# Kernel optimization log

Hardware: AMD Instinct MI355X
Metric: run time of the kernel (lower is better)

## Reference

```python
import jax, jax.numpy as jnp
import numpy as np

N, E, DIN, DOUT, NNZ = 8192, 4096, 256, 128, 65536
TEMP = float(DOUT) ** 0.5
NEG = -1e9


def setup_inputs() -> dict:
    key = jax.random.key(0)
    ks = jax.random.split(key, 8)
    stdv = 1.0 / np.sqrt(DOUT)
    u = lambda k, shp: jax.random.uniform(k, shp, jnp.float32, -stdv, stdv)
    x = jax.random.normal(ks[0], (N, DIN), jnp.float32)
    nodes = jax.random.randint(ks[1], (NNZ,), 0, N, jnp.int32)
    edges = jax.random.randint(ks[2], (NNZ,), 0, E, jnp.int32)
    hyperedge_index = jnp.stack([nodes, edges])  # [2, nnz]
    return {
        "x": x,
        "weight": u(ks[3], (DIN, DOUT)),   # transfer weight
        "weight2": u(ks[4], (DIN, DOUT)),
        "weight3": u(ks[5], (DOUT, DOUT)),
        "bias": u(ks[6], (DOUT,)),
        "q_ctx": u(ks[7], (DOUT,)),        # word_context.weight[0]
        "hyperedge_index": hyperedge_index,
        "num_nodes": N,
        "num_edges": E,
    }


def reference(x, weight, weight2, weight3, bias, q_ctx, hyperedge_index, num_nodes, num_edges):
    # dense incidence H[node, edge] = 1  (hyperedge_preprocess)
    H = jnp.zeros((num_nodes, num_edges), x.dtype).at[
        hyperedge_index[0], hyperedge_index[1]].set(1.0)
    adj = H.T                       # [E, N]  (mask / original attention for attn1)

    x4 = x @ weight2                # [N, D]  x_4att
    xt = x @ weight + bias          # [N, D]  transferred features (v of attn1)

    # ---- attention1: query = shared word-context vector, keys = x4 ----
    row = (q_ctx / TEMP) @ x4.T                    # [N] (q1 rows are identical)
    scores1 = jnp.where(adj == 0, NEG, row[None, :])  # [E, N]
    att1 = jax.nn.softmax(adj, axis=-1) + jax.nn.softmax(scores1, axis=-1)
    edge = att1 @ xt                               # [E, D]

    att2he = att1.T                                # [N, E]

    # ---- attention2: queries = x4, keys = edge @ W3 ----
    edge4 = edge @ weight3                         # [E, D]
    scores2 = jnp.where(adj.T == 0, NEG, (x4 / TEMP) @ edge4.T)  # [N, E]
    att2hn = jax.nn.softmax(adj.T, axis=-1) + jax.nn.softmax(scores2, axis=-1)

    # ---- fused outer-product attention and output projection ----
    A = att2he @ att2he.T + att2hn @ att2hn.T      # [N, N]
    h_prime_g = jax.nn.elu(A @ x4)                 # [N, D]
    return h_prime_g
```

## Files before the change

kernel.cpp:

```cpp
#include <hip/hip_runtime.h>
#include <math.h>

constexpr int Nn   = 8192;
constexpr int Ee   = 4096;
constexpr int DIN  = 256;
constexpr int DOUT = 128;
constexpr int NNZ  = 65536;
constexpr int EC   = 96;
constexpr int NC   = 48;

#define TEMPR 0.08838834764831845f
#define EM1   1.7182818284590452f

typedef __attribute__((ext_vector_type(8))) short short8;
typedef __attribute__((ext_vector_type(4))) float f32x4;

static __device__ __forceinline__ float wave_sum64(float v) {
#pragma unroll
    for (int m = 32; m; m >>= 1) v += __shfl_xor(v, m, 64);
    return v;
}
static __device__ __forceinline__ float wave_max64(float v) {
#pragma unroll
    for (int m = 32; m; m >>= 1) v = fmaxf(v, __shfl_xor(v, m, 64));
    return v;
}
static __device__ __forceinline__ short f2bf(float f) {
    union { float f; unsigned u; } v; v.f = f;
    const unsigned r = (v.u + 0x7FFFu + ((v.u >> 16) & 1u)) >> 16;
    return (short)r;
}
static __device__ __forceinline__ unsigned packbf2(float a, float b) {
    return ((unsigned)(unsigned short)f2bf(a)) |
           (((unsigned)(unsigned short)f2bf(b)) << 16);
}
static __device__ __forceinline__ float2 unpackbf2(unsigned u) {
    union { unsigned u; float f; } lo, hi;
    lo.u = u << 16; hi.u = u & 0xFFFF0000u;
    return make_float2(lo.f, hi.f);
}

__global__ __launch_bounds__(256) void k_ww3(
    const float* __restrict__ W, const float* __restrict__ W2,
    const float* __restrict__ W3, const float* __restrict__ bias,
    short* __restrict__ W2T, short* __restrict__ WWT, float* __restrict__ bW3,
    uint4* __restrict__ zb, unsigned zTot16)
{
    const int b = blockIdx.x;
    const int t = threadIdx.x;
    if (b < 32) {
        __shared__ float sW[8][128];
        const int r0 = b * 8;
        for (int i = t; i < 1024; i += 256)
            sW[i >> 7][i & 127] = W[(size_t)(r0 + (i >> 7)) * DOUT + (i & 127)];
        __syncthreads();
        const int c  = t & 127;
        const int rh = (t >> 7) * 4;
        float acc[4] = {0.f, 0.f, 0.f, 0.f};
        for (int k = 0; k < 128; ++k) {
            const float w3 = W3[(size_t)k * DOUT + c];
#pragma unroll
            for (int i = 0; i < 4; ++i) acc[i] = fmaf(sW[rh + i][k], w3, acc[i]);
        }
#pragma unroll
        for (int i = 0; i < 4; ++i)
            WWT[(size_t)c * DIN + (r0 + rh + i)] = f2bf(acc[i]);
    } else if (b < 40) {
        const int k0 = (b - 32) * 32;
        for (int i = t; i < 32 * 128; i += 256) {
            const int k = k0 + (i >> 7);
            const int n = i & 127;
            W2T[(size_t)n * DIN + k] = f2bf(W2[(size_t)k * DOUT + n]);
        }
    } else if (b == 40) {
        if (t < 128) {
            float acc = 0.f;
            for (int k = 0; k < 128; ++k)
                acc = fmaf(bias[k], W3[(size_t)k * DOUT + t], acc);
            bW3[t] = acc;
        }
    } else {
        uint4 z; z.x = z.y = z.z = z.w = 0u;
        for (unsigned i = (unsigned)(b - 41) * 256u + t; i < zTot16;
             i += 64u * 256u)
            zb[i] = z;
    }
}

__global__ __launch_bounds__(256) void k_gemm1f(
    const float* __restrict__ x, const short* __restrict__ W2T,
    const short* __restrict__ WWT, const float* __restrict__ bW3,
    const float* __restrict__ q, const int* __restrict__ hidx,
    unsigned* __restrict__ bitmap, int* __restrict__ degE, int* __restrict__ degN,
    int* __restrict__ csrEn, int* __restrict__ csrNe, int* __restrict__ csrNs,
    short* __restrict__ x4b, short* __restrict__ xwb,
    float* __restrict__ rowv)
{
    __shared__ float srow[16];
    const int t    = threadIdx.x;
    const int lane = t & 63;
    const int wv   = t >> 6;
    const int n16  = lane & 15;
    const int quad = lane >> 4;
    const int r0   = blockIdx.x * 16;
    const int n0   = wv * 32;

    const unsigned gid = blockIdx.x * 256 + t;
    if (gid < NNZ) {
        const int n = hidx[gid];
        const int e = hidx[NNZ + gid];
        const unsigned word = (unsigned)n * (unsigned)Ee + (unsigned)e;
        const unsigned bit  = 1u << (word & 31u);
        const unsigned old  = atomicOr(&bitmap[word >> 5], bit);
        if (!(old & bit)) {
            const int pe = atomicAdd(&degE[e], 1);
            if (pe < EC) {
                csrEn[e * EC + pe] = n;
                const int pn = atomicAdd(&degN[n], 1);
                if (pn < NC) {
                    csrNe[n * NC + pn] = e;
                    csrNs[n * NC + pn] = e * EC + pe;
                }
            }
        }
    }

    f32x4 acc4[2], accw[2];
#pragma unroll
    for (int nt = 0; nt < 2; ++nt) {
        acc4[nt] = (f32x4){0.f, 0.f, 0.f, 0.f};
        accw[nt] = (f32x4){0.f, 0.f, 0.f, 0.f};
    }
#pragma unroll
    for (int k0 = 0; k0 < DIN; k0 += 32) {
        const int kb = k0 + quad * 8;
        const float4 xa = *(const float4*)&x[(size_t)(r0 + n16) * DIN + kb];
        const float4 xb = *(const float4*)&x[(size_t)(r0 + n16) * DIN + kb + 4];
        short8 af;
        af[0] = f2bf(xa.x); af[1] = f2bf(xa.y); af[2] = f2bf(xa.z); af[3] = f2bf(xa.w);
        af[4] = f2bf(xb.x); af[5] = f2bf(xb.y); af[6] = f2bf(xb.z); af[7] = f2bf(xb.w);
#pragma unroll
        for (int nt = 0; nt < 2; ++nt) {
            const int col = n0 + nt * 16 + n16;
            const short8 b4 = *(const short8*)&W2T[(size_t)col * DIN + kb];
            const short8 bw = *(const short8*)&WWT[(size_t)col * DIN + kb];
            acc4[nt] = __builtin_amdgcn_mfma_f32_16x16x32_bf16(af, b4, acc4[nt], 0, 0, 0);
            accw[nt] = __builtin_amdgcn_mfma_f32_16x16x32_bf16(af, bw, accw[nt], 0, 0, 0);
        }
    }

    float bwv[2], qv[2];
#pragma unroll
    for (int nt = 0; nt < 2; ++nt) {
        const int col = n0 + nt * 16 + n16;
        bwv[nt] = bW3[col];
        qv[nt]  = q[col];
    }
#pragma unroll
    for (int nt = 0; nt < 2; ++nt) {
        const int col = n0 + nt * 16 + n16;
#pragma unroll
        for (int reg = 0; reg < 4; ++reg) {
            const int row = r0 + quad * 4 + reg;
            x4b[(size_t)row * DOUT + col] = f2bf(acc4[nt][reg]);
            xwb[(size_t)row * DOUT + col] = f2bf(accw[nt][reg] + bwv[nt]);
        }
    }
    float pr[4];
#pragma unroll
    for (int reg = 0; reg < 4; ++reg)
        pr[reg] = qv[0] * acc4[0][reg] + qv[1] * acc4[1][reg];
#pragma unroll
    for (int m = 8; m; m >>= 1) {
#pragma unroll
        for (int reg = 0; reg < 4; ++reg) pr[reg] += __shfl_xor(pr[reg], m, 64);
    }
    if (t < 16) srow[t] = 0.f;
    __syncthreads();
    if (n16 == 0) {
#pragma unroll
        for (int reg = 0; reg < 4; ++reg) atomicAdd(&srow[quad * 4 + reg], pr[reg]);
    }
    __syncthreads();
    if (t < 16) rowv[r0 + t] = srow[t] * TEMPR;
}

__global__ __launch_bounds__(256) void k_reduxA(
    const unsigned* __restrict__ x4b, const unsigned* __restrict__ xwb,
    const int* __restrict__ degE,
    float* __restrict__ csx4, float* __restrict__ csxw, float* __restrict__ c2g)
{
    const int t    = threadIdx.x;
    const int lane = t & 63;
    const int w    = t >> 6;
    const int b    = blockIdx.x;
    float2 a4 = {0.f, 0.f}, aw = {0.f, 0.f};
    for (int k = 0; k < 32; ++k) {
        const int n = b * 128 + w + k * 4;
        const float2 fv = unpackbf2(x4b[(size_t)n * 64 + lane]);
        const float2 tv = unpackbf2(xwb[(size_t)n * 64 + lane]);
        a4.x += fv.x; a4.y += fv.y;
        aw.x += tv.x; aw.y += tv.y;
    }
    atomicAdd(&csx4[lane * 2 + 0], a4.x); atomicAdd(&csx4[lane * 2 + 1], a4.y);
    atomicAdd(&csxw[lane * 2 + 0], aw.x); atomicAdd(&csxw[lane * 2 + 1], aw.y);

    const int gid = b * 256 + t;
    if (gid < Ee) {
        const int de = min(degE[gid], EC);
        const float ue = de ? 1.0f / ((float)Nn + (float)de * EM1)
                            : 2.0f / (float)Nn;
        const float v = wave_sum64(ue * ue);
        if (lane == 0) atomicAdd(c2g, v);
    }
}

__global__ __launch_bounds__(256) void k_edge1(
    const int* __restrict__ degE, const int* __restrict__ csrEn,
    const float* __restrict__ rowv,
    const float* __restrict__ csx4, const float* __restrict__ csxw,
    const unsigned* __restrict__ x4b, const unsigned* __restrict__ xwb,
    float* __restrict__ Sval, unsigned* __restrict__ e4b, unsigned* __restrict__ G1b,
    float* __restrict__ wsArr)
{
    __shared__ int   sN[4][EC];
    __shared__ float sS[4][EC];
    const int t    = threadIdx.x;
    const int w    = t >> 6;
    const int lane = t & 63;
    const int e    = blockIdx.x * 4 + w;
    const int deg  = min(degE[e], EC);
    const float ue = deg ? 1.0f / ((float)Nn + (float)deg * EM1) : 2.0f / (float)Nn;

    int   n0 = 0, n1 = 0;
    float r0 = -INFINITY, r1 = -INFINITY;
    if (lane < deg)      { n0 = csrEn[e * EC + lane];      r0 = rowv[n0]; }
    if (lane + 64 < deg) { n1 = csrEn[e * EC + lane + 64]; r1 = rowv[n1]; }
    const float m  = wave_max64(fmaxf(r0, r1));
    const float e0 = (lane < deg)      ? expf(r0 - m) : 0.f;
    const float e1 = (lane + 64 < deg) ? expf(r1 - m) : 0.f;
    const float Z  = wave_sum64(e0 + e1);
    const float inv = deg ? 1.0f / Z : 0.f;
    const float base = EM1 * ue;
    if (lane < deg) {
        const float sv = fmaf(e0, inv, base);
        sN[w][lane] = n0; sS[w][lane] = sv;
        Sval[e * EC + lane] = sv;
        atomicAdd(&wsArr[n0], ue * sv);
    }
    if (lane + 64 < deg) {
        const float sv = fmaf(e1, inv, base);
        sN[w][lane + 64] = n1; sS[w][lane + 64] = sv;
        Sval[e * EC + lane + 64] = sv;
        atomicAdd(&wsArr[n1], ue * sv);
    }

    const float2 cw = *(const float2*)&csxw[lane * 2];
    const float2 c4 = *(const float2*)&csx4[lane * 2];
    float2 aE = make_float2(ue * cw.x, ue * cw.y);
    float2 aG = make_float2(ue * c4.x, ue * c4.y);
    int j = 0;
    for (; j + 8 <= deg; j += 8) {
        int ai[8]; float bi[8]; unsigned tu[8], fu[8];
#pragma unroll
        for (int k = 0; k < 8; ++k) { ai[k] = sN[w][j+k]; bi[k] = sS[w][j+k]; }
#pragma unroll
        for (int k = 0; k < 8; ++k) {
            tu[k] = xwb[(size_t)ai[k] * 64 + lane];
            fu[k] = x4b[(size_t)ai[k] * 64 + lane];
        }
#pragma unroll
        for (int k = 0; k < 8; ++k) {
            const float2 tv = unpackbf2(tu[k]);
            const float2 fv = unpackbf2(fu[k]);
            aE.x = fmaf(bi[k], tv.x, aE.x); aE.y = fmaf(bi[k], tv.y, aE.y);
            aG.x = fmaf(bi[k], fv.x, aG.x); aG.y = fmaf(bi[k], fv.y, aG.y);
        }
    }
    for (; j < deg; ++j) {
        const int   a = sN[w][j];
        const float b = sS[w][j];
        const float2 tv = unpackbf2(xwb[(size_t)a * 64 + lane]);
        const float2 fv = unpackbf2(x4b[(size_t)a * 64 + lane]);
        aE.x = fmaf(b, tv.x, aE.x); aE.y = fmaf(b, tv.y, aE.y);
        aG.x = fmaf(b, fv.x, aG.x); aG.y = fmaf(b, fv.y, aG.y);
    }
    e4b[(size_t)e * 64 + lane] = packbf2(aE.x, aE.y);
    G1b[(size_t)e * 64 + lane] = packbf2(aG.x, aG.y);
}

__global__ __launch_bounds__(256) void k_reduxB(
    const unsigned* __restrict__ x4b, const int* __restrict__ degN,
    const float* __restrict__ wsArr,
    float* __restrict__ vxg, float* __restrict__ twxg, float* __restrict__ wsxg)
{
    const int t    = threadIdx.x;
    const int lane = t & 63;
    const int w    = t >> 6;
    const int b    = blockIdx.x;
    float2 av = {0.f, 0.f}, at2 = {0.f, 0.f}, aw = {0.f, 0.f};
    for (int k = 0; k < 32; ++k) {
        const int n   = b * 128 + w + k * 4;
        const int deg = min(degN[n], NC);
        const float vn = deg ? 1.0f / ((float)Ee + (float)deg * EM1) : 2.0f / (float)Ee;
        const float tw = deg ? fmaf((float)deg * EM1, vn, 1.0f) : 0.f;
        const float wsn = wsArr[n];
        const float2 xv = unpackbf2(x4b[(size_t)n * 64 + lane]);
        av.x  = fmaf(vn,  xv.x, av.x);  av.y  = fmaf(vn,  xv.y, av.y);
        at2.x = fmaf(tw,  xv.x, at2.x); at2.y = fmaf(tw,  xv.y, at2.y);
        aw.x  = fmaf(wsn, xv.x, aw.x);  aw.y  = fmaf(wsn, xv.y, aw.y);
    }
    atomicAdd(&vxg[lane * 2 + 0],  av.x);  atomicAdd(&vxg[lane * 2 + 1],  av.y);
    atomicAdd(&twxg[lane * 2 + 0], at2.x); atomicAdd(&twxg[lane * 2 + 1], at2.y);
    atomicAdd(&wsxg[lane * 2 + 0], aw.x);  atomicAdd(&wsxg[lane * 2 + 1], aw.y);
}

__global__ __launch_bounds__(256) void k_node2(
    const int* __restrict__ degN, const int* __restrict__ csrNe,
    const int* __restrict__ csrNs, const unsigned* __restrict__ x4b,
    const unsigned* __restrict__ e4b,
    float* __restrict__ Tval)
{
    const int t    = threadIdx.x;
    const int w    = t >> 6;
    const int lane = t & 63;
    const int es   = lane >> 3;
    const int dl   = lane & 7;
    const int n    = blockIdx.x * 4 + w;
    const int deg  = min(degN[n], NC);
    if (!deg) return;
    const float vn = 1.0f / ((float)Ee + (float)deg * EM1);

    const uint4* xr = (const uint4*)&x4b[(size_t)n * 64];
    const uint4 xua = xr[dl * 2], xub = xr[dl * 2 + 1];
    const float2 x0 = unpackbf2(xua.x), x1 = unpackbf2(xua.y),
                 x2 = unpackbf2(xua.z), x3 = unpackbf2(xua.w),
                 x4v = unpackbf2(xub.x), x5 = unpackbf2(xub.y),
                 x6 = unpackbf2(xub.z), x7 = unpackbf2(xub.w);

    float dps[6]; float exs[6]; int slots[6];
    float m = -INFINITY;
#pragma unroll
    for (int p = 0; p < 6; ++p) {
        dps[p] = -INFINITY; slots[p] = 0;
        if (p * 8 >= deg) continue;
        const int j = p * 8 + es;
        int ej = 0;
        if (j < deg) { ej = csrNe[n * NC + j]; slots[p] = csrNs[n * NC + j]; }
        const uint4* er = (const uint4*)&e4b[(size_t)ej * 64];
        const uint4 ea = er[dl * 2], eb = er[dl * 2 + 1];
        float d0 = 0.f, d1 = 0.f, d2 = 0.f, d3 = 0.f;
        { const float2 ev = unpackbf2(ea.x); d0 = fmaf(ev.x, x0.x, d0); d0 = fmaf(ev.y, x0.y, d0); }
        { const float2 ev = unpackbf2(ea.y); d1 = fmaf(ev.x, x1.x, d1); d1 = fmaf(ev.y, x1.y, d1); }
        { const float2 ev = unpackbf2(ea.z); d2 = fmaf(ev.x, x2.x, d2); d2 = fmaf(ev.y, x2.y, d2); }
        { const float2 ev = unpackbf2(ea.w); d3 = fmaf(ev.x, x3.x, d3); d3 = fmaf(ev.y, x3.y, d3); }
        { const float2 ev = unpackbf2(eb.x); d0 = fmaf(ev.x, x4v.x, d0); d0 = fmaf(ev.y, x4v.y, d0); }
        { const float2 ev = unpackbf2(eb.y); d1 = fmaf(ev.x, x5.x, d1); d1 = fmaf(ev.y, x5.y, d1); }
        { const float2 ev = unpackbf2(eb.z); d2 = fmaf(ev.x, x6.x, d2); d2 = fmaf(ev.y, x6.y, d2); }
        { const float2 ev = unpackbf2(eb.w); d3 = fmaf(ev.x, x7.x, d3); d3 = fmaf(ev.y, x7.y, d3); }
        float dot = (d0 + d1) + (d2 + d3);
        dot += __shfl_xor(dot, 1, 64);
        dot += __shfl_xor(dot, 2, 64);
        dot += __shfl_xor(dot, 4, 64);
        dot = (j < deg) ? dot * TEMPR : -INFINITY;
        dps[p] = dot;
        float mm = fmaxf(dot, __shfl_xor(dot, 8, 64));
        mm = fmaxf(mm, __shfl_xor(mm, 16, 64));
        mm = fmaxf(mm, __shfl_xor(mm, 32, 64));
        m = fmaxf(m, mm);
    }
    float Z = 0.f;
#pragma unroll
    for (int p = 0; p < 6; ++p) {
        exs[p] = 0.f;
        if (p * 8 >= deg) continue;
        const float ex = (p * 8 + es < deg) ? expf(dps[p] - m) : 0.f;
        exs[p] = ex;
        float s = ex + __shfl_xor(ex, 8, 64);
        s += __shfl_xor(s, 16, 64);
        s += __shfl_xor(s, 32, 64);
        Z += s;
    }
    const float invZ = 1.0f / Z;
#pragma unroll
    for (int p = 0; p < 6; ++p) {
        if (p * 8 >= deg) continue;
        if (dl == 0 && p * 8 + es < deg)
            Tval[slots[p]] = fmaf(EM1, vn, exs[p] * invZ);
    }
}

__global__ __launch_bounds__(256) void k_g2(
    const int* __restrict__ degE, const int* __restrict__ csrEn,
    const float* __restrict__ Tval, const float* __restrict__ vxg,
    const unsigned* __restrict__ x4b, unsigned* __restrict__ G2b)
{
    const int t    = threadIdx.x;
    const int w    = t >> 6;
    const int lane = t & 63;
    const int e    = blockIdx.x * 4 + w;
    const int deg  = min(degE[e], EC);
    float2 acc = *(const float2*)&vxg[lane * 2];
    int j = 0;
    for (; j + 8 <= deg; j += 8) {
        int ai[8]; float bi[8]; unsigned fu[8];
#pragma unroll
        for (int k = 0; k < 8; ++k) { ai[k] = csrEn[e*EC+j+k]; bi[k] = Tval[e*EC+j+k]; }
#pragma unroll
        for (int k = 0; k < 8; ++k)
            fu[k] = x4b[(size_t)ai[k] * 64 + lane];
#pragma unroll
        for (int k = 0; k < 8; ++k) {
            const float2 fv = unpackbf2(fu[k]);
            acc.x = fmaf(bi[k], fv.x, acc.x); acc.y = fmaf(bi[k], fv.y, acc.y);
        }
    }
    for (; j < deg; ++j) {
        const int   a = csrEn[e*EC+j];
        const float b = Tval[e*EC+j];
        const float2 fv = unpackbf2(x4b[(size_t)a * 64 + lane]);
        acc.x = fmaf(b, fv.x, acc.x); acc.y = fmaf(b, fv.y, acc.y);
    }
    G2b[(size_t)e * 64 + lane] = packbf2(acc.x, acc.y);
}

__global__ __launch_bounds__(256) void k_final(
    const int* __restrict__ degN, const int* __restrict__ csrNe,
    const int* __restrict__ csrNs, const float* __restrict__ Sval,
    const float* __restrict__ Tval,
    const float* __restrict__ c2g, const float* __restrict__ csx4,
    const float* __restrict__ wsxg, const float* __restrict__ vxg,
    const float* __restrict__ twxg,
    const unsigned* __restrict__ G1b, const unsigned* __restrict__ G2b,
    float* __restrict__ out)
{
    const int t    = threadIdx.x;
    const int w    = t >> 6;
    const int lane = t & 63;
    const int n    = blockIdx.x * 4 + w;
    const int deg  = min(degN[n], NC);
    const float vn = deg ? 1.0f / ((float)Ee + (float)deg * EM1) : 2.0f / (float)Ee;
    const float c2 = *c2g;
    const float2 c4v = *(const float2*)&csx4[lane * 2];
    const float2 wsv = *(const float2*)&wsxg[lane * 2];
    const float2 vxv = *(const float2*)&vxg[lane * 2];
    const float2 twv = *(const float2*)&twxg[lane * 2];
    float2 acc;
    acc.x = fmaf(c2, c4v.x, wsv.x) + vn * fmaf((float)Ee, vxv.x, twv.x);
    acc.y = fmaf(c2, c4v.y, wsv.y) + vn * fmaf((float)Ee, vxv.y, twv.y);
    int j = 0;
    for (; j + 4 <= deg; j += 4) {
        int ei[4], si[4]; float sv[4], tv[4]; unsigned g1u[4], g2u[4];
#pragma unroll
        for (int k = 0; k < 4; ++k) {
            ei[k] = csrNe[n*NC+j+k]; si[k] = csrNs[n*NC+j+k];
        }
#pragma unroll
        for (int k = 0; k < 4; ++k) {
            sv[k] = Sval[si[k]]; tv[k] = Tval[si[k]];
            g1u[k] = G1b[(size_t)ei[k] * 64 + lane];
            g2u[k] = G2b[(size_t)ei[k] * 64 + lane];
        }
#pragma unroll
        for (int k = 0; k < 4; ++k) {
            const float2 g1 = unpackbf2(g1u[k]);
            const float2 g2 = unpackbf2(g2u[k]);
            acc.x = fmaf(sv[k], g1.x, acc.x); acc.y = fmaf(sv[k], g1.y, acc.y);
            acc.x = fmaf(tv[k], g2.x, acc.x); acc.y = fmaf(tv[k], g2.y, acc.y);
        }
    }
    for (; j < deg; ++j) {
        const int ea = csrNe[n*NC+j];
        const int sa = csrNs[n*NC+j];
        const float sva = Sval[sa], tva = Tval[sa];
        const float2 g1a = unpackbf2(G1b[(size_t)ea * 64 + lane]);
        const float2 g2a = unpackbf2(G2b[(size_t)ea * 64 + lane]);
        acc.x = fmaf(sva, g1a.x, acc.x); acc.y = fmaf(sva, g1a.y, acc.y);
        acc.x = fmaf(tva, g2a.x, acc.x); acc.y = fmaf(tva, g2a.y, acc.y);
    }
    acc.x = acc.x > 0.f ? acc.x : expm1f(acc.x);
    acc.y = acc.y > 0.f ? acc.y : expm1f(acc.y);
    *(float2*)&out[(size_t)n * DOUT + lane * 2] = acc;
}

extern "C" void kernel_launch(void* const* d_in, const int* in_sizes, int n_in,
                              void* d_out, int out_size, void* d_ws, size_t ws_size,
                              hipStream_t stream)
{
    const float* x    = (const float*)d_in[0];
    const float* W    = (const float*)d_in[1];
    const float* W2   = (const float*)d_in[2];
    const float* W3   = (const float*)d_in[3];
    const float* bias = (const float*)d_in[4];
    const float* q    = (const float*)d_in[5];
    const int*   hidx = (const int*)d_in[6];
    float* out = (float*)d_out;

    char* wsp = (char*)d_ws;
    size_t o = 0;
    auto take = [&](size_t bytes) {
        size_t r = o; o += (bytes + 255) & ~(size_t)255; return r;
    };
    unsigned* bitmap = (unsigned*)(wsp + take((size_t)Nn * Ee / 8));
    int*   degE  = (int*)  (wsp + take((size_t)Ee * 4));
    int*   degN  = (int*)  (wsp + take((size_t)Nn * 4));
    float* wsArr = (float*)(wsp + take((size_t)Nn * 4));
    float* c2g   = (float*)(wsp + take(4));
    float* csx4  = (float*)(wsp + take(DOUT * 4));
    float* csxw  = (float*)(wsp + take(DOUT * 4));
    float* vxg   = (float*)(wsp + take(DOUT * 4));
    float* twxg  = (float*)(wsp + take(DOUT * 4));
    float* wsxg  = (float*)(wsp + take(DOUT * 4));
    const size_t zbytes = o;
    short* x4b   = (short*)(wsp + take((size_t)Nn * DOUT * 2));
    short* xwb   = (short*)(wsp + take((size_t)Nn * DOUT * 2));
    float* rowv  = (float*)(wsp + take((size_t)Nn * 4));
    int*   csrEn = (int*)  (wsp + take((size_t)Ee * EC * 4));
    float* Sval  = (float*)(wsp + take((size_t)Ee * EC * 4));
    float* Tval  = (float*)(wsp + take((size_t)Ee * EC * 4));
    int*   csrNe = (int*)  (wsp + take((size_t)Nn * NC * 4));
    int*   csrNs = (int*)  (wsp + take((size_t)Nn * NC * 4));
    unsigned* e4b = (unsigned*)(wsp + take((size_t)Ee * DOUT * 2));
    unsigned* G1b = (unsigned*)(wsp + take((size_t)Ee * DOUT * 2));
    unsigned* G2b = (unsigned*)(wsp + take((size_t)Ee * DOUT * 2));
    short* W2T   = (short*)(wsp + take((size_t)DOUT * DIN * 2));
    short* WWT   = (short*)(wsp + take((size_t)DOUT * DIN * 2));
    float* bW3   = (float*)(wsp + take(DOUT * 4));
    (void)ws_size; (void)in_sizes; (void)n_in; (void)out_size;

    k_ww3   <<<105,     256, 0, stream>>>(W, W2, W3, bias, W2T, WWT, bW3,
                                          (uint4*)d_ws, (unsigned)(zbytes / 16));
    k_gemm1f<<<Nn / 16, 256, 0, stream>>>(x, W2T, WWT, bW3, q, hidx,
                                          bitmap, degE, degN, csrEn, csrNe, csrNs,
                                          x4b, xwb, rowv);
    k_reduxA<<<64,      256, 0, stream>>>((const unsigned*)x4b, (const unsigned*)xwb,
                                          degE, csx4, csxw, c2g);
    k_edge1 <<<Ee / 4,  256, 0, stream>>>(degE, csrEn, rowv, csx4, csxw,
                                          (const unsigned*)x4b, (const unsigned*)xwb,
                                          Sval, e4b, G1b, wsArr);
    k_reduxB<<<64,      256, 0, stream>>>((const unsigned*)x4b, degN, wsArr,
                                          vxg, twxg, wsxg);
    k_node2 <<<Nn / 4,  256, 0, stream>>>(degN, csrNe, csrNs,
                                          (const unsigned*)x4b, e4b, Tval);
    k_g2    <<<Ee / 4,  256, 0, stream>>>(degE, csrEn, Tval, vxg,
                                          (const unsigned*)x4b, G2b);
    k_final <<<Nn / 4,  256, 0, stream>>>(degN, csrNe, csrNs, Sval, Tval,
                                          c2g, csx4, wsxg, vxg, twxg, G1b, G2b, out);
}
```

Baseline: 167.1 us.

## Interleave per-slot and per-row arrays into packed structs and merge reduction kernel

Packs the separate node-index, S and T arrays into one int4 per edge slot, and the node CSR edge/slot pair into an int2. It interleaves x4 and xw bf16 rows, and G1 and G2, so each gather fetches one 8-byte word instead of two 4-byte loads. The column order is permuted so the GEMM epilogue can pack adjacent outputs, and k_final un-permutes the layout on store. It also folds the k_reduxB reduction into the k_nodeB launch as extra blocks and deepens the edge gather unroll to 16. The intent is fewer scattered memory transactions and one fewer launch, at the cost of wider per-slot records and a duplicated x4 copy.

```diff
diff --git a/kernel.cpp b/kernel.cpp
--- a/kernel.cpp
+++ b/kernel.cpp
@@ -11,6 +11,7 @@
 
 #define TEMPR 0.08838834764831845f
 #define EM1   1.7182818284590452f
+
 
 typedef __attribute__((ext_vector_type(8))) short short8;
 typedef __attribute__((ext_vector_type(4))) float f32x4;
@@ -92,8 +93,8 @@
     const short* __restrict__ WWT, const float* __restrict__ bW3,
     const float* __restrict__ q, const int* __restrict__ hidx,
     unsigned* __restrict__ bitmap, int* __restrict__ degE, int* __restrict__ degN,
-    int* __restrict__ csrEn, int* __restrict__ csrNe, int* __restrict__ csrNs,
-    short* __restrict__ x4b, short* __restrict__ xwb,
+    int4* __restrict__ EST, int2* __restrict__ csrNES,
+    uint2* __restrict__ xfb, unsigned* __restrict__ x4s,
     float* __restrict__ rowv)
 {
     __shared__ float srow[16];
@@ -115,12 +116,10 @@
         if (!(old & bit)) {
             const int pe = atomicAdd(&degE[e], 1);
             if (pe < EC) {
-                csrEn[e * EC + pe] = n;
+                EST[e * EC + pe].x = n;
                 const int pn = atomicAdd(&degN[n], 1);
-                if (pn < NC) {
-                    csrNe[n * NC + pn] = e;
-                    csrNs[n * NC + pn] = e * EC + pe;
-                }
+                if (pn < NC)
+                    csrNES[n * NC + pn] = make_int2(e, e * EC + pe);
             }
         }
     }
@@ -156,15 +155,15 @@
         bwv[nt] = bW3[col];
         qv[nt]  = q[col];
     }
-#pragma unroll
-    for (int nt = 0; nt < 2; ++nt) {
-        const int col = n0 + nt * 16 + n16;
-#pragma unroll
-        for (int reg = 0; reg < 4; ++reg) {
-            const int row = r0 + quad * 4 + reg;
-            x4b[(size_t)row * DOUT + col] = f2bf(acc4[nt][reg]);
-            xwb[(size_t)row * DOUT + col] = f2bf(accw[nt][reg] + bwv[nt]);
-        }
+    const int s = wv * 16 + n16;
+#pragma unroll
+    for (int reg = 0; reg < 4; ++reg) {
+        const int row = r0 + quad * 4 + reg;
+        uint2 v;
+        v.x = packbf2(acc4[0][reg], acc4[1][reg]);
+        v.y = packbf2(accw[0][reg] + bwv[0], accw[1][reg] + bwv[1]);
+        xfb[(size_t)row * 64 + s] = v;
+        x4s[(size_t)row * 64 + s] = v.x;
     }
     float pr[4];
 #pragma unroll
@@ -186,9 +185,8 @@
 }
 
 __global__ __launch_bounds__(256) void k_reduxA(
-    const unsigned* __restrict__ x4b, const unsigned* __restrict__ xwb,
-    const int* __restrict__ degE,
-    float* __restrict__ csx4, float* __restrict__ csxw, float* __restrict__ c2g)
+    const uint2* __restrict__ xfb, const int* __restrict__ degE,
+    float* __restrict__ csAB, float* __restrict__ c2g)
 {
     const int t    = threadIdx.x;
     const int lane = t & 63;
@@ -197,13 +195,14 @@
     float2 a4 = {0.f, 0.f}, aw = {0.f, 0.f};
     for (int k = 0; k < 32; ++k) {
         const int n = b * 128 + w + k * 4;
-        const float2 fv = unpackbf2(x4b[(size_t)n * 64 + lane]);
-        const float2 tv = unpackbf2(xwb[(size_t)n * 64 + lane]);
+        const uint2 u = xfb[(size_t)n * 64 + lane];
+        const float2 fv = unpackbf2(u.x);
+        const float2 tv = unpackbf2(u.y);
         a4.x += fv.x; a4.y += fv.y;
         aw.x += tv.x; aw.y += tv.y;
     }
-    atomicAdd(&csx4[lane * 2 + 0], a4.x); atomicAdd(&csx4[lane * 2 + 1], a4.y);
-    atomicAdd(&csxw[lane * 2 + 0], aw.x); atomicAdd(&csxw[lane * 2 + 1], aw.y);
+    atomicAdd(&csAB[lane * 4 + 0], a4.x); atomicAdd(&csAB[lane * 4 + 1], a4.y);
+    atomicAdd(&csAB[lane * 4 + 2], aw.x); atomicAdd(&csAB[lane * 4 + 3], aw.y);
 
     const int gid = b * 256 + t;
     if (gid < Ee) {
@@ -216,11 +215,10 @@
 }
 
 __global__ __launch_bounds__(256) void k_edge1(
-    const int* __restrict__ degE, const int* __restrict__ csrEn,
-    const float* __restrict__ rowv,
-    const float* __restrict__ csx4, const float* __restrict__ csxw,
-    const unsigned* __restrict__ x4b, const unsigned* __restrict__ xwb,
-    float* __restrict__ Sval, unsigned* __restrict__ e4b, unsigned* __restrict__ G1b,
+    const int* __restrict__ degE, int4* __restrict__ EST,
+    const float* __restrict__ rowv, const float* __restrict__ csAB,
+    const uint2* __restrict__ xfb,
+    unsigned* __restrict__ e4b, uint2* __restrict__ GG,
     float* __restrict__ wsArr)
 {
     __shared__ int   sN[4][EC];
@@ -234,8 +232,8 @@
 
     int   n0 = 0, n1 = 0;
     float r0 = -INFINITY, r1 = -INFINITY;
-    if (lane < deg)      { n0 = csrEn[e * EC + lane];      r0 = rowv[n0]; }
-    if (lane + 64 < deg) { n1 = csrEn[e * EC + lane + 64]; r1 = rowv[n1]; }
+    if (lane < deg)      { n0 = EST[e * EC + lane].x;      r0 = rowv[n0]; }
+    if (lane + 64 < deg) { n1 = EST[e * EC + lane + 64].x; r1 = rowv[n1]; }
     const float m  = wave_max64(fmaxf(r0, r1));
     const float e0 = (lane < deg)      ? expf(r0 - m) : 0.f;
     const float e1 = (lane + 64 < deg) ? expf(r1 - m) : 0.f;
@@ -245,34 +243,44 @@
     if (lane < deg) {
         const float sv = fmaf(e0, inv, base);
         sN[w][lane] = n0; sS[w][lane] = sv;
-        Sval[e * EC + lane] = sv;
+        EST[e * EC + lane].y = __float_as_int(sv);
         atomicAdd(&wsArr[n0], ue * sv);
     }
     if (lane + 64 < deg) {
         const float sv = fmaf(e1, inv, base);
         sN[w][lane + 64] = n1; sS[w][lane + 64] = sv;
-        Sval[e * EC + lane + 64] = sv;
+        EST[e * EC + lane + 64].y = __float_as_int(sv);
         atomicAdd(&wsArr[n1], ue * sv);
     }
 
-    const float2 cw = *(const float2*)&csxw[lane * 2];
-    const float2 c4 = *(const float2*)&csx4[lane * 2];
-    float2 aE = make_float2(ue * cw.x, ue * cw.y);
-    float2 aG = make_float2(ue * c4.x, ue * c4.y);
+    const float4 cs = *(const float4*)&csAB[lane * 4];
+    float2 aE = make_float2(ue * cs.z, ue * cs.w);
+    float2 aG = make_float2(ue * cs.x, ue * cs.y);
     int j = 0;
+    for (; j + 16 <= deg; j += 16) {
+        int ai[16]; float bi[16]; uint2 fu[16];
+#pragma unroll
+        for (int k = 0; k < 16; ++k) { ai[k] = sN[w][j+k]; bi[k] = sS[w][j+k]; }
+#pragma unroll
+        for (int k = 0; k < 16; ++k) fu[k] = xfb[(size_t)ai[k] * 64 + lane];
+#pragma unroll
+        for (int k = 0; k < 16; ++k) {
+            const float2 fv = unpackbf2(fu[k].x);
+            const float2 tv = unpackbf2(fu[k].y);
+            aE.x = fmaf(bi[k], tv.x, aE.x); aE.y = fmaf(bi[k], tv.y, aE.y);
+            aG.x = fmaf(bi[k], fv.x, aG.x); aG.y = fmaf(bi[k], fv.y, aG.y);
+        }
+    }
     for (; j + 8 <= deg; j += 8) {
-        int ai[8]; float bi[8]; unsigned tu[8], fu[8];
+        int ai[8]; float bi[8]; uint2 fu[8];
 #pragma unroll
         for (int k = 0; k < 8; ++k) { ai[k] = sN[w][j+k]; bi[k] = sS[w][j+k]; }
 #pragma unroll
+        for (int k = 0; k < 8; ++k) fu[k] = xfb[(size_t)ai[k] * 64 + lane];
+#pragma unroll
         for (int k = 0; k < 8; ++k) {
-            tu[k] = xwb[(size_t)ai[k] * 64 + lane];
-            fu[k] = x4b[(size_t)ai[k] * 64 + lane];
-        }
-#pragma unroll
-        for (int k = 0; k < 8; ++k) {
-            const float2 tv = unpackbf2(tu[k]);
-            const float2 fv = unpackbf2(fu[k]);
+            const float2 fv = unpackbf2(fu[k].x);
+            const float2 tv = unpackbf2(fu[k].y);
             aE.x = fmaf(bi[k], tv.x, aE.x); aE.y = fmaf(bi[k], tv.y, aE.y);
             aG.x = fmaf(bi[k], fv.x, aG.x); aG.y = fmaf(bi[k], fv.y, aG.y);
         }
@@ -280,58 +288,55 @@
     for (; j < deg; ++j) {
         const int   a = sN[w][j];
         const float b = sS[w][j];
-        const float2 tv = unpackbf2(xwb[(size_t)a * 64 + lane]);
-        const float2 fv = unpackbf2(x4b[(size_t)a * 64 + lane]);
+        const uint2 u = xfb[(size_t)a * 64 + lane];
+        const float2 fv = unpackbf2(u.x);
+        const float2 tv = unpackbf2(u.y);
         aE.x = fmaf(b, tv.x, aE.x); aE.y = fmaf(b, tv.y, aE.y);
         aG.x = fmaf(b, fv.x, aG.x); aG.y = fmaf(b, fv.y, aG.y);
     }
     e4b[(size_t)e * 64 + lane] = packbf2(aE.x, aE.y);
-    G1b[(size_t)e * 64 + lane] = packbf2(aG.x, aG.y);
-}
-
-__global__ __launch_bounds__(256) void k_reduxB(
-    const unsigned* __restrict__ x4b, const int* __restrict__ degN,
-    const float* __restrict__ wsArr,
-    float* __restrict__ vxg, float* __restrict__ twxg, float* __restrict__ wsxg)
-{
-    const int t    = threadIdx.x;
-    const int lane = t & 63;
-    const int w    = t >> 6;
-    const int b    = blockIdx.x;
-    float2 av = {0.f, 0.f}, at2 = {0.f, 0.f}, aw = {0.f, 0.f};
-    for (int k = 0; k < 32; ++k) {
-        const int n   = b * 128 + w + k * 4;
-        const int deg = min(degN[n], NC);
-        const float vn = deg ? 1.0f / ((float)Ee + (float)deg * EM1) : 2.0f / (float)Ee;
-        const float tw = deg ? fmaf((float)deg * EM1, vn, 1.0f) : 0.f;
-        const float wsn = wsArr[n];
-        const float2 xv = unpackbf2(x4b[(size_t)n * 64 + lane]);
-        av.x  = fmaf(vn,  xv.x, av.x);  av.y  = fmaf(vn,  xv.y, av.y);
-        at2.x = fmaf(tw,  xv.x, at2.x); at2.y = fmaf(tw,  xv.y, at2.y);
-        aw.x  = fmaf(wsn, xv.x, aw.x);  aw.y  = fmaf(wsn, xv.y, aw.y);
-    }
-    atomicAdd(&vxg[lane * 2 + 0],  av.x);  atomicAdd(&vxg[lane * 2 + 1],  av.y);
-    atomicAdd(&twxg[lane * 2 + 0], at2.x); atomicAdd(&twxg[lane * 2 + 1], at2.y);
-    atomicAdd(&wsxg[lane * 2 + 0], aw.x);  atomicAdd(&wsxg[lane * 2 + 1], aw.y);
-}
-
-__global__ __launch_bounds__(256) void k_node2(
-    const int* __restrict__ degN, const int* __restrict__ csrNe,
-    const int* __restrict__ csrNs, const unsigned* __restrict__ x4b,
-    const unsigned* __restrict__ e4b,
-    float* __restrict__ Tval)
+    GG[(size_t)e * 64 + lane].x = packbf2(aG.x, aG.y);
+}
+
+__global__ __launch_bounds__(256) void k_nodeB(
+    const int* __restrict__ degN, const int2* __restrict__ csrNES,
+    const unsigned* __restrict__ x4s, const unsigned* __restrict__ e4b,
+    const float* __restrict__ wsArr, int4* __restrict__ EST,
+    float* __restrict__ vxg2, float* __restrict__ twg2, float* __restrict__ wsg2)
 {
     const int t    = threadIdx.x;
     const int w    = t >> 6;
     const int lane = t & 63;
+    const int b    = blockIdx.x;
+
+    if (b < 64) {
+        float2 av = {0.f, 0.f}, at2 = {0.f, 0.f}, aw = {0.f, 0.f};
+        for (int k = 0; k < 32; ++k) {
+            const int n   = b * 128 + w + k * 4;
+            const int deg = min(degN[n], NC);
+            const float vn = deg ? 1.0f / ((float)Ee + (float)deg * EM1)
+                                 : 2.0f / (float)Ee;
+            const float tw = deg ? fmaf((float)deg * EM1, vn, 1.0f) : 0.f;
+            const float wsn = wsArr[n];
+            const float2 xv = unpackbf2(x4s[(size_t)n * 64 + lane]);
+            av.x  = fmaf(vn,  xv.x, av.x);  av.y  = fmaf(vn,  xv.y, av.y);
+            at2.x = fmaf(tw,  xv.x, at2.x); at2.y = fmaf(tw,  xv.y, at2.y);
+            aw.x  = fmaf(wsn, xv.x, aw.x);  aw.y  = fmaf(wsn, xv.y, aw.y);
+        }
+        atomicAdd(&vxg2[lane*2+0], av.x);  atomicAdd(&vxg2[lane*2+1], av.y);
+        atomicAdd(&twg2[lane*2+0], at2.x); atomicAdd(&twg2[lane*2+1], at2.y);
+        atomicAdd(&wsg2[lane*2+0], aw.x);  atomicAdd(&wsg2[lane*2+1], aw.y);
+        return;
+    }
+
     const int es   = lane >> 3;
     const int dl   = lane & 7;
-    const int n    = blockIdx.x * 4 + w;
+    const int n    = (b - 64) * 4 + w;
     const int deg  = min(degN[n], NC);
     if (!deg) return;
     const float vn = 1.0f / ((float)Ee + (float)deg * EM1);
 
-    const uint4* xr = (const uint4*)&x4b[(size_t)n * 64];
+    const uint4* xr = (const uint4*)&x4s[(size_t)n * 64];
     const uint4 xua = xr[dl * 2], xub = xr[dl * 2 + 1];
     const float2 x0 = unpackbf2(xua.x), x1 = unpackbf2(xua.y),
                  x2 = unpackbf2(xua.z), x3 = unpackbf2(xua.w),
@@ -346,7 +351,10 @@
         if (p * 8 >= deg) continue;
         const int j = p * 8 + es;
         int ej = 0;
-        if (j < deg) { ej = csrNe[n * NC + j]; slots[p] = csrNs[n * NC + j]; }
+        if (j < deg) {
+            const int2 en = csrNES[n * NC + j];
+            ej = en.x; slots[p] = en.y;
+        }
         const uint4* er = (const uint4*)&e4b[(size_t)ej * 64];
         const uint4 ea = er[dl * 2], eb = er[dl * 2 + 1];
         float d0 = 0.f, d1 = 0.f, d2 = 0.f, d3 = 0.f;
@@ -376,63 +384,62 @@
         if (p * 8 >= deg) continue;
         const float ex = (p * 8 + es < deg) ? expf(dps[p] - m) : 0.f;
         exs[p] = ex;
-        float s = ex + __shfl_xor(ex, 8, 64);
-        s += __shfl_xor(s, 16, 64);
-        s += __shfl_xor(s, 32, 64);
-        Z += s;
+        float sum = ex + __shfl_xor(ex, 8, 64);
+        sum += __shfl_xor(sum, 16, 64);
+        sum += __shfl_xor(sum, 32, 64);
+        Z += sum;
     }
     const float invZ = 1.0f / Z;
 #pragma unroll
     for (int p = 0; p < 6; ++p) {
         if (p * 8 >= deg) continue;
         if (dl == 0 && p * 8 + es < deg)
-            Tval[slots[p]] = fmaf(EM1, vn, exs[p] * invZ);
+            EST[slots[p]].z = __float_as_int(fmaf(EM1, vn, exs[p] * invZ));
     }
 }
 
 __global__ __launch_bounds__(256) void k_g2(
-    const int* __restrict__ degE, const int* __restrict__ csrEn,
-    const float* __restrict__ Tval, const float* __restrict__ vxg,
-    const unsigned* __restrict__ x4b, unsigned* __restrict__ G2b)
+    const int* __restrict__ degE, const int4* __restrict__ EST,
+    const float* __restrict__ vxg2, const unsigned* __restrict__ x4s,
+    uint2* __restrict__ GG)
 {
     const int t    = threadIdx.x;
     const int w    = t >> 6;
     const int lane = t & 63;
     const int e    = blockIdx.x * 4 + w;
     const int deg  = min(degE[e], EC);
-    float2 acc = *(const float2*)&vxg[lane * 2];
+    float2 acc = *(const float2*)&vxg2[lane * 2];
     int j = 0;
     for (; j + 8 <= deg; j += 8) {
-        int ai[8]; float bi[8]; unsigned fu[8];
-#pragma unroll
-        for (int k = 0; k < 8; ++k) { ai[k] = csrEn[e*EC+j+k]; bi[k] = Tval[e*EC+j+k]; }
+        int4 st[8]; unsigned fu[8];
+#pragma unroll
+        for (int k = 0; k < 8; ++k) st[k] = EST[e * EC + j + k];
 #pragma unroll
         for (int k = 0; k < 8; ++k)
-            fu[k] = x4b[(size_t)ai[k] * 64 + lane];
+            fu[k] = x4s[(size_t)st[k].x * 64 + lane];
 #pragma unroll
         for (int k = 0; k < 8; ++k) {
+            const float  bt = __int_as_float(st[k].z);
             const float2 fv = unpackbf2(fu[k]);
-            acc.x = fmaf(bi[k], fv.x, acc.x); acc.y = fmaf(bi[k], fv.y, acc.y);
+            acc.x = fmaf(bt, fv.x, acc.x); acc.y = fmaf(bt, fv.y, acc.y);
         }
     }
     for (; j < deg; ++j) {
-        const int   a = csrEn[e*EC+j];
-        const float b = Tval[e*EC+j];
-        const float2 fv = unpackbf2(x4b[(size_t)a * 64 + lane]);
-        acc.x = fmaf(b, fv.x, acc.x); acc.y = fmaf(b, fv.y, acc.y);
-    }
-    G2b[(size_t)e * 64 + lane] = packbf2(acc.x, acc.y);
+        const int4 st = EST[e * EC + j];
+        const float bt = __int_as_float(st.z);
+        const float2 fv = unpackbf2(x4s[(size_t)st.x * 64 + lane]);
+        acc.x = fmaf(bt, fv.x, acc.x); acc.y = fmaf(bt, fv.y, acc.y);
+    }
+    GG[(size_t)e * 64 + lane].y = packbf2(acc.x, acc.y);
 }
 
 __global__ __launch_bounds__(256) void k_final(
-    const int* __restrict__ degN, const int* __restrict__ csrNe,
-    const int* __restrict__ csrNs, const float* __restrict__ Sval,
-    const float* __restrict__ Tval,
-    const float* __restrict__ c2g, const float* __restrict__ csx4,
-    const float* __restrict__ wsxg, const float* __restrict__ vxg,
-    const float* __restrict__ twxg,
-    const unsigned* __restrict__ G1b, const unsigned* __restrict__ G2b,
-    float* __restrict__ out)
+    const int* __restrict__ degN, const int2* __restrict__ csrNES,
+    const int4* __restrict__ EST,
+    const float* __restrict__ c2g, const float* __restrict__ csAB,
+    const float* __restrict__ wsg2, const float* __restrict__ vxg2,
+    const float* __restrict__ twg2,
+    const uint2* __restrict__ GG, float* __restrict__ out)
 {
     const int t    = threadIdx.x;
     const int w    = t >> 6;
@@ -441,46 +448,49 @@
     const int deg  = min(degN[n], NC);
     const float vn = deg ? 1.0f / ((float)Ee + (float)deg * EM1) : 2.0f / (float)Ee;
     const float c2 = *c2g;
-    const float2 c4v = *(const float2*)&csx4[lane * 2];
-    const float2 wsv = *(const float2*)&wsxg[lane * 2];
-    const float2 vxv = *(const float2*)&vxg[lane * 2];
-    const float2 twv = *(const float2*)&twxg[lane * 2];
+    const float2 c4v = *(const float2*)&csAB[lane * 4];
+    const float2 wsv = *(const float2*)&wsg2[lane * 2];
+    const float2 vxv = *(const float2*)&vxg2[lane * 2];
+    const float2 twv = *(const float2*)&twg2[lane * 2];
     float2 acc;
     acc.x = fmaf(c2, c4v.x, wsv.x) + vn * fmaf((float)Ee, vxv.x, twv.x);
     acc.y = fmaf(c2, c4v.y, wsv.y) + vn * fmaf((float)Ee, vxv.y, twv.y);
     int j = 0;
-    for (; j + 4 <= deg; j += 4) {
-        int ei[4], si[4]; float sv[4], tv[4]; unsigned g1u[4], g2u[4];
-#pragma unroll
-        for (int k = 0; k < 4; ++k) {
-            ei[k] = csrNe[n*NC+j+k]; si[k] = csrNs[n*NC+j+k];
-        }
-#pragma unroll
-        for (int k = 0; k < 4; ++k) {
-            sv[k] = Sval[si[k]]; tv[k] = Tval[si[k]];
-            g1u[k] = G1b[(size_t)ei[k] * 64 + lane];
-            g2u[k] = G2b[(size_t)ei[k] * 64 + lane];
-        }
-#pragma unroll
-        for (int k = 0; k < 4; ++k) {
-            const float2 g1 = unpackbf2(g1u[k]);
-            const float2 g2 = unpackbf2(g2u[k]);
-            acc.x = fmaf(sv[k], g1.x, acc.x); acc.y = fmaf(sv[k], g1.y, acc.y);
-            acc.x = fmaf(tv[k], g2.x, acc.x); acc.y = fmaf(tv[k], g2.y, acc.y);
+    for (; j + 8 <= deg; j += 8) {
+        int2 es[8]; int4 st[8]; uint2 gg[8];
+#pragma unroll
+        for (int k = 0; k < 8; ++k) es[k] = csrNES[n * NC + j + k];
+#pragma unroll
+        for (int k = 0; k < 8; ++k) {
+            st[k] = EST[es[k].y];
+            gg[k] = GG[(size_t)es[k].x * 64 + lane];
+        }
+#pragma unroll
+        for (int k = 0; k < 8; ++k) {
+            const float sva = __int_as_float(st[k].y);
+            const float tva = __int_as_float(st[k].z);
+            const float2 g1 = unpackbf2(gg[k].x);
+            const float2 g2 = unpackbf2(gg[k].y);
+            acc.x = fmaf(sva, g1.x, acc.x); acc.y = fmaf(sva, g1.y, acc.y);
+            acc.x = fmaf(tva, g2.x, acc.x); acc.y = fmaf(tva, g2.y, acc.y);
         }
     }
     for (; j < deg; ++j) {
-        const int ea = csrNe[n*NC+j];
-        const int sa = csrNs[n*NC+j];
-        const float sva = Sval[sa], tva = Tval[sa];
-        const float2 g1a = unpackbf2(G1b[(size_t)ea * 64 + lane]);
-        const float2 g2a = unpackbf2(G2b[(size_t)ea * 64 + lane]);
-        acc.x = fmaf(sva, g1a.x, acc.x); acc.y = fmaf(sva, g1a.y, acc.y);
-        acc.x = fmaf(tva, g2a.x, acc.x); acc.y = fmaf(tva, g2a.y, acc.y);
+        const int2 es = csrNES[n * NC + j];
+        const int4 st = EST[es.y];
+        const uint2 gg = GG[(size_t)es.x * 64 + lane];
+        const float sva = __int_as_float(st.y);
+        const float tva = __int_as_float(st.z);
+        const float2 g1 = unpackbf2(gg.x);
+        const float2 g2 = unpackbf2(gg.y);
+        acc.x = fmaf(sva, g1.x, acc.x); acc.y = fmaf(sva, g1.y, acc.y);
+        acc.x = fmaf(tva, g2.x, acc.x); acc.y = fmaf(tva, g2.y, acc.y);
     }
     acc.x = acc.x > 0.f ? acc.x : expm1f(acc.x);
     acc.y = acc.y > 0.f ? acc.y : expm1f(acc.y);
-    *(float2*)&out[(size_t)n * DOUT + lane * 2] = acc;
+    const int lo = ((lane >> 4) << 5) + (lane & 15);
+    out[(size_t)n * DOUT + lo]      = acc.x;
+    out[(size_t)n * DOUT + lo + 16] = acc.y;
 }
 
 extern "C" void kernel_launch(void* const* d_in, const int* in_sizes, int n_in,
@@ -506,44 +516,34 @@
     int*   degN  = (int*)  (wsp + take((size_t)Nn * 4));
     float* wsArr = (float*)(wsp + take((size_t)Nn * 4));
     float* c2g   = (float*)(wsp + take(4));
-    float* csx4  = (float*)(wsp + take(DOUT * 4));
-    float* csxw  = (float*)(wsp + take(DOUT * 4));
-    float* vxg   = (float*)(wsp + take(DOUT * 4));
-    float* twxg  = (float*)(wsp + take(DOUT * 4));
-    float* wsxg  = (float*)(wsp + take(DOUT * 4));
+    float* csAB  = (float*)(wsp + take(64 * 16));
+    float* vxg2  = (float*)(wsp + take(DOUT * 4));
+    float* twg2  = (float*)(wsp + take(DOUT * 4));
+    float* wsg2  = (float*)(wsp + take(DOUT * 4));
     const size_t zbytes = o;
-    short* x4b   = (short*)(wsp + take((size_t)Nn * DOUT * 2));
-    short* xwb   = (short*)(wsp + take((size_t)Nn * DOUT * 2));
-    float* rowv  = (float*)(wsp + take((size_t)Nn * 4));
-    int*   csrEn = (int*)  (wsp + take((size_t)Ee * EC * 4));
-    float* Sval  = (float*)(wsp + take((size_t)Ee * EC * 4));
-    float* Tval  = (float*)(wsp + take((size_t)Ee * EC * 4));
-    int*   csrNe = (int*)  (wsp + take((size_t)Nn * NC * 4));
-    int*   csrNs = (int*)  (wsp + take((size_t)Nn * NC * 4));
-    unsigned* e4b = (unsigned*)(wsp + take((size_t)Ee * DOUT * 2));
-    unsigned* G1b = (unsigned*)(wsp + take((size_t)Ee * DOUT * 2));
-    unsigned* G2b = (unsigned*)(wsp + take((size_t)Ee * DOUT * 2));
-    short* W2T   = (short*)(wsp + take((size_t)DOUT * DIN * 2));
-    short* WWT   = (short*)(wsp + take((size_t)DOUT * DIN * 2));
-    float* bW3   = (float*)(wsp + take(DOUT * 4));
+    uint2*    xfb    = (uint2*)   (wsp + take((size_t)Nn * 64 * 8));
+    unsigned* x4s    = (unsigned*)(wsp + take((size_t)Nn * 64 * 4));
+    float*    rowv   = (float*)   (wsp + take((size_t)Nn * 4));
+    int4*     EST    = (int4*)    (wsp + take((size_t)Ee * EC * 16));
+    int2*     csrNES = (int2*)    (wsp + take((size_t)Nn * NC * 8));
+    unsigned* e4b    = (unsigned*)(wsp + take((size_t)Ee * 64 * 4));
+    uint2*    GG     = (uint2*)   (wsp + take((size_t)Ee * 64 * 8));
+    short*    W2T    = (short*)   (wsp + take((size_t)DOUT * DIN * 2));
+    short*    WWT    = (short*)   (wsp + take((size_t)DOUT * DIN * 2));
+    float*    bW3    = (float*)   (wsp + take(DOUT * 4));
     (void)ws_size; (void)in_sizes; (void)n_in; (void)out_size;
 
-    k_ww3   <<<105,     256, 0, stream>>>(W, W2, W3, bias, W2T, WWT, bW3,
-                                          (uint4*)d_ws, (unsigned)(zbytes / 16));
-    k_gemm1f<<<Nn / 16, 256, 0, stream>>>(x, W2T, WWT, bW3, q, hidx,
-                                          bitmap, degE, degN, csrEn, csrNe, csrNs,
-                                          x4b, xwb, rowv);
-    k_reduxA<<<64,      256, 0, stream>>>((const unsigned*)x4b, (const unsigned*)xwb,
-                                          degE, csx4, csxw, c2g);
-    k_edge1 <<<Ee / 4,  256, 0, stream>>>(degE, csrEn, rowv, csx4, csxw,
-                                          (const unsigned*)x4b, (const unsigned*)xwb,
-                                          Sval, e4b, G1b, wsArr);
-    k_reduxB<<<64,      256, 0, stream>>>((const unsigned*)x4b, degN, wsArr,
-                                          vxg, twxg, wsxg);
-    k_node2 <<<Nn / 4,  256, 0, stream>>>(degN, csrNe, csrNs,
-                                          (const unsigned*)x4b, e4b, Tval);
-    k_g2    <<<Ee / 4,  256, 0, stream>>>(degE, csrEn, Tval, vxg,
-                                          (const unsigned*)x4b, G2b);
-    k_final <<<Nn / 4,  256, 0, stream>>>(degN, csrNe, csrNs, Sval, Tval,
-                                          c2g, csx4, wsxg, vxg, twxg, G1b, G2b, out);
-}
+    k_ww3   <<<105,        256, 0, stream>>>(W, W2, W3, bias, W2T, WWT, bW3,
+                                             (uint4*)d_ws, (unsigned)(zbytes / 16));
+    k_gemm1f<<<Nn / 16,    256, 0, stream>>>(x, W2T, WWT, bW3, q, hidx,
+                                             bitmap, degE, degN, EST, csrNES,
+                                             xfb, x4s, rowv);
+    k_reduxA<<<64,         256, 0, stream>>>(xfb, degE, csAB, c2g);
+    k_edge1 <<<Ee / 4,     256, 0, stream>>>(degE, EST, rowv, csAB, xfb,
+                                             e4b, GG, wsArr);
+    k_nodeB <<<64 + Nn/4,  256, 0, stream>>>(degN, csrNES, x4s, e4b, wsArr,
+                                             EST, vxg2, twg2, wsg2);
+    k_g2    <<<Ee / 4,     256, 0, stream>>>(degE, EST, vxg2, x4s, GG);
+    k_final <<<Nn / 4,     256, 0, stream>>>(degN, csrNES, EST, c2g, csAB,
+                                             wsg2, vxg2, twg2, GG, out);
+}
```

Measured after the change: 181.3 us. +8.5%, slower.
